# Optimization experiments

Hardware: AMD Instinct MI355X
Metric: run time of the kernel (lower is better)

## Reference

```python
import jax, jax.numpy as jnp
import numpy as np

D_MODEL = 1024
N_HEADS = 16
D_HEAD = D_MODEL // N_HEADS


def setup_inputs() -> dict:
    key = jax.random.key(0)
    k1, k2, k3 = jax.random.split(key, 3)
    B, T = 2, 2048
    x = jax.random.normal(k1, (B, T, D_MODEL), dtype=jnp.float32)
    # kaiming_normal fan_out on torch Linear weight [out, in]: std = sqrt(2/out)
    qkv_w = jax.random.normal(k2, (3 * D_MODEL, D_MODEL), dtype=jnp.float32) * np.sqrt(2.0 / (3 * D_MODEL)).astype(np.float32)
    out_w = jax.random.normal(k3, (D_MODEL, D_MODEL), dtype=jnp.float32) * np.sqrt(2.0 / D_MODEL).astype(np.float32)
    return {"x": x, "qkv_w": qkv_w, "out_w": out_w}


def rotate_half(x):
    x1, x2 = x[..., : x.shape[-1] // 2], x[..., x.shape[-1] // 2 :]
    return jnp.concatenate((-x2, x1), axis=-1)


def reference(x, qkv_w, out_w):
    B, T, D = x.shape
    H, dh = N_HEADS, D_HEAD
    scale = dh ** -0.5

    qkv = jnp.einsum('btd,ed->bte', x, qkv_w)  # [B,T,3D]
    q, k, v = jnp.split(qkv, 3, axis=-1)
    # [B,H,T,dh]
    q = q.reshape(B, T, H, dh).transpose(0, 2, 1, 3)
    k = k.reshape(B, T, H, dh).transpose(0, 2, 1, 3)
    v = v.reshape(B, T, H, dh).transpose(0, 2, 1, 3)

    # rotary embeddings
    inv_freq = 1.0 / (10000.0 ** (jnp.arange(0, dh, 2, dtype=jnp.float32) / dh))
    t = jnp.arange(T, dtype=jnp.float32)
    freqs = jnp.einsum('i,j->ij', t, inv_freq)        # [T, dh/2]
    emb = jnp.concatenate((freqs, freqs), axis=-1)    # [T, dh]
    cos = jnp.cos(emb)[None, None]                    # [1,1,T,dh]
    sin = jnp.sin(emb)[None, None]
    q = q * cos + rotate_half(q) * sin
    k = k * cos + rotate_half(k) * sin

    scores = jnp.einsum('bhqd,bhkd->bhqk', q, k) * scale
    causal = jnp.tril(jnp.ones((T, T), dtype=bool))
    scores = jnp.where(causal, scores, -jnp.inf)
    attn = jax.nn.softmax(scores, axis=-1)
    out = jnp.einsum('bhqk,bhkd->bhqd', attn, v)      # [B,H,T,dh]
    out = out.transpose(0, 2, 1, 3).reshape(B, T, D)
    return jnp.einsum('btd,ed->bte', out, out_w)
```

## Files before the change

kernel.cpp:

```cpp
#include <hip/hip_runtime.h>
#include <hip/hip_bf16.h>
#include <cmath>

#define Bb   2
#define Tseq 2048
#define NH   16
#define DM   1024

using f32x4 = __attribute__((ext_vector_type(4))) float;
using s16x8 = __attribute__((ext_vector_type(8))) short;
using s16x4 = __attribute__((ext_vector_type(4))) short;

typedef const __attribute__((address_space(1))) unsigned char* as1p;
typedef __attribute__((address_space(3))) unsigned char* as3p;

static __device__ __forceinline__ void gload_lds16(const void* g, void* l){
  __builtin_amdgcn_global_load_lds((as1p)g, (as3p)l, 16, 0, 0);
}

#if defined(__has_builtin)
#if __has_builtin(__builtin_amdgcn_mfma_f32_16x16x16bf16_1k)
#define MFMA16(acc, va, pb) (acc) = __builtin_amdgcn_mfma_f32_16x16x16bf16_1k((va), (pb), (acc), 0, 0, 0)
#endif
#endif
#ifndef MFMA16
#define MFMA16(acc, va, pb) asm volatile("s_nop 1\n\tv_mfma_f32_16x16x16_bf16 %0, %1, %2, %0" : "+v"(acc) : "v"(va), "v"(pb))
#endif

static __device__ __forceinline__ float b2f(unsigned short u){
  union { unsigned int u; float f; } v; v.u = ((unsigned int)u) << 16; return v.f;
}
static __device__ __forceinline__ unsigned short f2b(float f){
  union { float f; unsigned int u; } v; v.f = f;
  unsigned int u = v.u;
  return (unsigned short)((u + 0x7fffu + ((u >> 16) & 1u)) >> 16);
}

__global__ void k_convert(const float* __restrict__ in, unsigned short* __restrict__ out, int n){
  int stride = gridDim.x * blockDim.x;
  for (int i = blockIdx.x * blockDim.x + threadIdx.x; i * 4 < n; i += stride) {
    const float4 v = *reinterpret_cast<const float4*>(in + (size_t)i * 4);
    ushort4 o; o.x = f2b(v.x); o.y = f2b(v.y); o.z = f2b(v.z); o.w = f2b(v.w);
    *reinterpret_cast<ushort4*>(out + (size_t)i * 4) = o;
  }
}

__global__ void k_tables(float* __restrict__ cosT, float* __restrict__ sinT){
  int idx = blockIdx.x * blockDim.x + threadIdx.x;
  int t = idx >> 5, j = idx & 31;
  float invf = __powf(10000.0f, -(float)j / 32.0f);
  float a = (float)t * invf;
  cosT[idx] = cosf(a);
  sinT[idx] = sinf(a);
}

template<int OUT_BF16>
__global__ __launch_bounds__(256) void k_gemm_bt(const unsigned short* __restrict__ A,
                                                 const unsigned short* __restrict__ W,
                                                 void* __restrict__ Cout,
                                                 int M, int N, int K, int NYL){
  __shared__ unsigned short As[128*32];
  __shared__ unsigned short Bs[128*32];
  const int i = (int)blockIdx.x;
  const int xcd = i & 7, r = i >> 3;
  const int bx = r / NYL, by = xcd * NYL + (r % NYL);
  const int bm = bx * 128, bn = by * 128;
  const int tid = threadIdx.x;
  const int lane = tid & 63, w = tid >> 6;
  const int wr = w >> 1, wc = w & 1;
  const int g = lane >> 4, ln = lane & 15;
  f32x4 acc[4][4] = {};
  char* asb = (char*)As + w * 2048;
  char* bsb = (char*)Bs + w * 2048;
  const int lrow = lane >> 2;
  const int kcol = (lane & 3) * 8;
  const size_t aro = (size_t)(bm + w * 32 + lrow) * K;
  const size_t bro = (size_t)(bn + w * 32 + lrow) * K;
  for (int k0 = 0; k0 < K; k0 += 32) {
    gload_lds16(A + aro + k0 + kcol,                  asb);
    gload_lds16(A + aro + (size_t)16 * K + k0 + kcol, asb + 1024);
    gload_lds16(W + bro + k0 + kcol,                  bsb);
    gload_lds16(W + bro + (size_t)16 * K + k0 + kcol, bsb + 1024);
    __syncthreads();
    s16x8 af[4], bfr[4];
    #pragma unroll
    for (int mt = 0; mt < 4; ++mt)
      af[mt] = *reinterpret_cast<const s16x8*>(&As[(wr*64 + mt*16 + ln)*32 + g*8]);
    #pragma unroll
    for (int nt = 0; nt < 4; ++nt)
      bfr[nt] = *reinterpret_cast<const s16x8*>(&Bs[(wc*64 + nt*16 + ln)*32 + g*8]);
    #pragma unroll
    for (int mt = 0; mt < 4; ++mt)
      #pragma unroll
      for (int nt = 0; nt < 4; ++nt)
        acc[mt][nt] = __builtin_amdgcn_mfma_f32_16x16x32_bf16(af[mt], bfr[nt], acc[mt][nt], 0, 0, 0);
    __syncthreads();
  }
  #pragma unroll
  for (int mt = 0; mt < 4; ++mt)
    #pragma unroll
    for (int nt = 0; nt < 4; ++nt)
      #pragma unroll
      for (int r2 = 0; r2 < 4; ++r2) {
        int row = bm + wr*64 + mt*16 + g*4 + r2;
        int col = bn + wc*64 + nt*16 + ln;
        float vv = acc[mt][nt][r2];
        if (OUT_BF16) reinterpret_cast<unsigned short*>(Cout)[(size_t)row * N + col] = f2b(vv);
        else          reinterpret_cast<float*>(Cout)[(size_t)row * N + col] = vv;
      }
}

__global__ __launch_bounds__(256) void k_rope_split(const unsigned short* __restrict__ qkv,
                                                    const float* __restrict__ cosT,
                                                    const float* __restrict__ sinT,
                                                    unsigned short* __restrict__ qr,
                                                    unsigned short* __restrict__ kr){
  int bt = blockIdx.x;
  int b = bt / Tseq, t = bt % Tseq;
  const unsigned short* row = qkv + (size_t)bt * 3072;
  for (int d = threadIdx.x; d < 1024; d += 256) {
    int h = d >> 6, dd = d & 63;
    int j = dd & 31;
    float c = cosT[t*32 + j], s = sinT[t*32 + j];
    int part = (dd < 32) ? (d + 32) : (d - 32);
    float xq  = b2f(row[d]);
    float xq2 = b2f(row[part]);
    float qv = (dd < 32) ? (xq*c - xq2*s) : (xq*c + xq2*s);
    size_t head_off = ((size_t)(b*NH + h) * Tseq + t) * 64 + dd;
    qr[head_off] = f2b(qv * 0.125f);
    float xk  = b2f(row[1024 + d]);
    float xk2 = b2f(row[1024 + part]);
    float kv = (dd < 32) ? (xk*c - xk2*s) : (xk*c + xk2*s);
    kr[head_off] = f2b(kv);
  }
}

__global__ __launch_bounds__(256) void k_vtrans(const unsigned short* __restrict__ qkv,
                                                unsigned short* __restrict__ vt){
  __shared__ unsigned short L[64*72];
  const int blk = blockIdx.x;
  const int tt64 = blk & 31, bh = blk >> 5;
  const int b = bh >> 4, h = bh & 15;
  const int t0 = tt64 * 64;
  const int tid = threadIdx.x;
  {
    const int tr = tid >> 2, c = tid & 3;
    const unsigned short* src = qkv + ((size_t)(b * Tseq) + t0 + tr) * 3072 + 2048 + h * 64 + c * 16;
    uint4 a0 = *reinterpret_cast<const uint4*>(src);
    uint4 a1 = *reinterpret_cast<const uint4*>(src + 8);
    *reinterpret_cast<uint4*>(&L[tr * 72 + c * 16])     = a0;
    *reinterpret_cast<uint4*>(&L[tr * 72 + c * 16 + 8]) = a1;
  }
  __syncthreads();
  {
    const int d = tid >> 2, c = tid & 3;
    unsigned int wq[8];
    #pragma unroll
    for (int j = 0; j < 8; ++j) {
      unsigned int lo = L[(c * 16 + 2 * j)     * 72 + d];
      unsigned int hi = L[(c * 16 + 2 * j + 1) * 72 + d];
      wq[j] = lo | (hi << 16);
    }
    unsigned short* dst = vt + ((size_t)bh * 64 + d) * Tseq + t0 + c * 16;
    *reinterpret_cast<uint4*>(dst)     = make_uint4(wq[0], wq[1], wq[2], wq[3]);
    *reinterpret_cast<uint4*>(dst + 8) = make_uint4(wq[4], wq[5], wq[6], wq[7]);
  }
}

__global__ __launch_bounds__(256, 2) void k_attn(const unsigned short* __restrict__ Qr,
                                                 const unsigned short* __restrict__ Kr,
                                                 const unsigned short* __restrict__ Vt,
                                                 unsigned short* __restrict__ Ao){
  __shared__ unsigned short Ks[2][64*64];
  __shared__ unsigned short Vs[2][64*64];
  __shared__ unsigned short Ps[4][16*72];
  const int i = (int)blockIdx.x;
  const int xcd = i & 7, r = i >> 3;
  const int bh = xcd * 4 + (r >> 4);
  const int pj = r & 15;
  const unsigned short* Q  = Qr + (size_t)bh * Tseq * 64;
  const unsigned short* Kp = Kr + (size_t)bh * Tseq * 64;
  const unsigned short* Vp = Vt + (size_t)bh * 64 * Tseq;
  const int tid = threadIdx.x;
  const int w = tid >> 6, lane = tid & 63;
  const int g = lane >> 4, ln = lane & 15;
  const int srow = tid >> 2;
  const int c2 = (tid & 3) * 2;
  const int wb0 = srow * 128 + ((c2 * 16)        ^ ((srow & 7) << 4));
  const int wb1 = srow * 128 + ((c2 * 16 + 16)   ^ ((srow & 7) << 4));
  const int scol = c2 * 8;
  const int x0 = (g * 16)      ^ ((ln & 7) << 4);
  const int x1 = (64 + g * 16) ^ ((ln & 7) << 4);
  unsigned short* Pw = Ps[w];
  const int b = bh / NH, h = bh % NH;

  #pragma unroll
  for (int pass = 0; pass < 2; ++pass) {
    const int j = pass ? (31 - pj) : pj;
    const int q0 = j * 64;
    const int ntiles = j + 1;
    const int q0w = q0 + w * 16;

    s16x8 qf0 = *reinterpret_cast<const s16x8*>(&Q[(size_t)(q0w + ln) * 64 + g * 8]);
    s16x8 qf1 = *reinterpret_cast<const s16x8*>(&Q[(size_t)(q0w + ln) * 64 + 32 + g * 8]);

    f32x4 oacc[4] = {};
    float lsum = 0.f;

    {
      uint4 k0 = *reinterpret_cast<const uint4*>(&Kp[(size_t)srow * 64 + scol]);
      uint4 k1 = *reinterpret_cast<const uint4*>(&Kp[(size_t)srow * 64 + scol + 8]);
      uint4 v0 = *reinterpret_cast<const uint4*>(&Vp[(size_t)srow * Tseq + scol]);
      uint4 v1 = *reinterpret_cast<const uint4*>(&Vp[(size_t)srow * Tseq + scol + 8]);
      *reinterpret_cast<uint4*>((char*)Ks[0] + wb0) = k0;
      *reinterpret_cast<uint4*>((char*)Ks[0] + wb1) = k1;
      *reinterpret_cast<uint4*>((char*)Vs[0] + wb0) = v0;
      *reinterpret_cast<uint4*>((char*)Vs[0] + wb1) = v1;
    }
    __syncthreads();
    int cur = 0;

    for (int kt = 0; kt < ntiles; ++kt) {
      const bool pre = (kt + 1 < ntiles);
      uint4 nk0, nk1, nv0, nv1;
      if (pre) {
        const unsigned short* gk = &Kp[(size_t)((kt + 1) * 64 + srow) * 64 + scol];
        const unsigned short* gv = &Vp[(size_t)srow * Tseq + (kt + 1) * 64 + scol];
        nk0 = *reinterpret_cast<const uint4*>(gk);
        nk1 = *reinterpret_cast<const uint4*>(gk + 8);
        nv0 = *reinterpret_cast<const uint4*>(gv);
        nv1 = *reinterpret_cast<const uint4*>(gv + 8);
      }
      f32x4 s[4] = {};
      const char* kb = (const char*)Ks[cur];
      __builtin_amdgcn_s_setprio(1);
      #pragma unroll
      for (int nt = 0; nt < 4; ++nt) {
        s16x8 kfa = *reinterpret_cast<const s16x8*>(kb + nt * 2048 + ln * 128 + x0);
        s16x8 kfb = *reinterpret_cast<const s16x8*>(kb + nt * 2048 + ln * 128 + x1);
        s[nt] = __builtin_amdgcn_mfma_f32_16x16x32_bf16(kfa, qf0, s[nt], 0, 0, 0);
        s[nt] = __builtin_amdgcn_mfma_f32_16x16x32_bf16(kfb, qf1, s[nt], 0, 0, 0);
      }
      __builtin_amdgcn_s_setprio(0);
      if (kt == ntiles - 1) {
        #pragma unroll
        for (int nt = 0; nt < 4; ++nt)
          #pragma unroll
          for (int r2 = 0; r2 < 4; ++r2)
            if (nt * 16 + g * 4 + r2 > w * 16 + ln) s[nt][r2] = -1e30f;
      }
      s16x4 pb[4];
      #pragma unroll
      for (int nt = 0; nt < 4; ++nt)
        #pragma unroll
        for (int r2 = 0; r2 < 4; ++r2) {
          float p = __expf(s[nt][r2]);
          lsum += p;
          pb[nt][r2] = (short)f2b(p);
        }
      const char* vb = (const char*)Vs[cur];
      __builtin_amdgcn_s_setprio(1);
      #pragma unroll
      for (int dt = 0; dt < 4; ++dt) {
        #pragma unroll
        for (int nt = 0; nt < 4; ++nt) {
          s16x4 va = *reinterpret_cast<const s16x4*>(vb + (dt * 16 + ln) * 128 + ((nt * 32 + g * 8) ^ ((ln & 7) << 4)));
          MFMA16(oacc[dt], va, pb[nt]);
        }
      }
      __builtin_amdgcn_s_setprio(0);
      if (pre) {
        const int nxt = cur ^ 1;
        *reinterpret_cast<uint4*>((char*)Ks[nxt] + wb0) = nk0;
        *reinterpret_cast<uint4*>((char*)Ks[nxt] + wb1) = nk1;
        *reinterpret_cast<uint4*>((char*)Vs[nxt] + wb0) = nv0;
        *reinterpret_cast<uint4*>((char*)Vs[nxt] + wb1) = nv1;
      }
      __syncthreads();
      cur ^= 1;
    }

    float l = lsum;
    l += __shfl_xor(l, 16);
    l += __shfl_xor(l, 32);
    float inv = 1.f / l;
    #pragma unroll
    for (int nt = 0; nt < 4; ++nt) {
      unsigned int lo = (unsigned int)f2b(oacc[nt][0] * inv) | ((unsigned int)f2b(oacc[nt][1] * inv) << 16);
      unsigned int hi = (unsigned int)f2b(oacc[nt][2] * inv) | ((unsigned int)f2b(oacc[nt][3] * inv) << 16);
      *reinterpret_cast<uint2*>(&Pw[ln * 72 + nt * 16 + g * 4]) = make_uint2(lo, hi);
    }
    asm volatile("s_waitcnt lgkmcnt(0)" ::: "memory");
    __builtin_amdgcn_sched_barrier(0);
    const int rr = lane >> 2;
    const int cc = (lane & 3) * 8;
    uint4 ov0 = *reinterpret_cast<const uint4*>(&Pw[rr * 72 + cc]);
    uint4 ov1 = *reinterpret_cast<const uint4*>(&Pw[rr * 72 + cc + 32]);
    int t = q0w + rr;
    unsigned short* orow = &Ao[((size_t)(b * Tseq + t) * DM) + h * 64];
    *reinterpret_cast<uint4*>(orow + cc)      = ov0;
    *reinterpret_cast<uint4*>(orow + cc + 32) = ov1;
  }
}

extern "C" void kernel_launch(void* const* d_in, const int* in_sizes, int n_in,
                              void* d_out, int out_size, void* d_ws, size_t ws_size,
                              hipStream_t stream) {
  const float* x    = (const float*)d_in[0];
  const float* qkvw = (const float*)d_in[1];
  const float* outw = (const float*)d_in[2];
  float* out = (float*)d_out;
  char* ws = (char*)d_ws;
  size_t off = 0;
  auto alloc = [&](size_t bytes)->void*{ void* p = ws + off; off += (bytes + 255) & ~(size_t)255; return p; };
  unsigned short* x_bf   = (unsigned short*)alloc((size_t)Bb*Tseq*DM*2);
  unsigned short* qw_bf  = (unsigned short*)alloc((size_t)3*DM*DM*2);
  unsigned short* ow_bf  = (unsigned short*)alloc((size_t)DM*DM*2);
  float*          cosT   = (float*)alloc((size_t)Tseq*32*4);
  float*          sinT   = (float*)alloc((size_t)Tseq*32*4);
  unsigned short* qkv_bf = (unsigned short*)alloc((size_t)Bb*Tseq*3*DM*2);
  unsigned short* qr     = (unsigned short*)alloc((size_t)Bb*NH*Tseq*64*2);
  unsigned short* kr     = (unsigned short*)alloc((size_t)Bb*NH*Tseq*64*2);
  unsigned short* vt     = (unsigned short*)alloc((size_t)Bb*NH*Tseq*64*2);
  unsigned short* ao     = (unsigned short*)alloc((size_t)Bb*Tseq*DM*2);
  (void)ws_size; (void)in_sizes; (void)n_in; (void)out_size;

  const int nx  = Bb*Tseq*DM;
  const int nqw = 3*DM*DM;
  const int now = DM*DM;
  k_convert<<<2048, 256, 0, stream>>>(x, x_bf, nx);
  k_convert<<<2048, 256, 0, stream>>>(qkvw, qw_bf, nqw);
  k_convert<<<1024, 256, 0, stream>>>(outw, ow_bf, now);
  k_tables<<<256, 256, 0, stream>>>(cosT, sinT);
  k_gemm_bt<1><<<768, 256, 0, stream>>>(x_bf, qw_bf, qkv_bf, Bb*Tseq, 3*DM, DM, 3);
  k_rope_split<<<Bb*Tseq, 256, 0, stream>>>(qkv_bf, cosT, sinT, qr, kr);
  k_vtrans<<<Bb*NH*(Tseq/64), 256, 0, stream>>>(qkv_bf, vt);
  k_attn<<<dim3(Bb*NH*16), 256, 0, stream>>>(qr, kr, vt, ao);
  k_gemm_bt<0><<<256, 256, 0, stream>>>(ao, ow_bf, out, Bb*Tseq, DM, DM, 1);
}
```

Baseline: 131.3 us.

## Fuse RoPE and head split into QKV GEMM epilogue; deepen K tile with swizzled LDS

The QKV GEMM epilogue now applies rotary embedding, the Q scale and the per-head layout directly from accumulators. This removes the separate rope_split kernel and its extra read and write of the Q/K portion of the qkv buffer. Only the V region is still written to the qkv buffer. The GEMM K-step is also doubled to 64 with an XOR-swizzled LDS layout to cut barrier count and bank conflicts. In exchange, LDS use is doubled and the epilogue loads cos/sin tables per row.

```diff
diff --git a/kernel.cpp b/kernel.cpp
--- a/kernel.cpp
+++ b/kernel.cpp
@@ -54,84 +54,105 @@
   sinT[idx] = sinf(a);
 }
 
-template<int OUT_BF16>
+template<int MODE>
 __global__ __launch_bounds__(256) void k_gemm_bt(const unsigned short* __restrict__ A,
                                                  const unsigned short* __restrict__ W,
                                                  void* __restrict__ Cout,
-                                                 int M, int N, int K, int NYL){
-  __shared__ unsigned short As[128*32];
-  __shared__ unsigned short Bs[128*32];
+                                                 int M, int N, int K, int NYL,
+                                                 const float* __restrict__ cosT,
+                                                 const float* __restrict__ sinT,
+                                                 unsigned short* __restrict__ qr,
+                                                 unsigned short* __restrict__ kr){
+  __shared__ unsigned short As[128*64];
+  __shared__ unsigned short Bs[128*64];
   const int i = (int)blockIdx.x;
-  const int xcd = i & 7, r = i >> 3;
-  const int bx = r / NYL, by = xcd * NYL + (r % NYL);
+  const int xcd = i & 7, rr = i >> 3;
+  const int bx = rr / NYL, by = xcd * NYL + (rr % NYL);
   const int bm = bx * 128, bn = by * 128;
   const int tid = threadIdx.x;
   const int lane = tid & 63, w = tid >> 6;
   const int wr = w >> 1, wc = w & 1;
   const int g = lane >> 4, ln = lane & 15;
   f32x4 acc[4][4] = {};
-  char* asb = (char*)As + w * 2048;
-  char* bsb = (char*)Bs + w * 2048;
-  const int lrow = lane >> 2;
-  const int kcol = (lane & 3) * 8;
-  const size_t aro = (size_t)(bm + w * 32 + lrow) * K;
-  const size_t bro = (size_t)(bn + w * 32 + lrow) * K;
-  for (int k0 = 0; k0 < K; k0 += 32) {
-    gload_lds16(A + aro + k0 + kcol,                  asb);
-    gload_lds16(A + aro + (size_t)16 * K + k0 + kcol, asb + 1024);
-    gload_lds16(W + bro + k0 + kcol,                  bsb);
-    gload_lds16(W + bro + (size_t)16 * K + k0 + kcol, bsb + 1024);
+  char* asb = (char*)As + w * 4096;
+  char* bsb = (char*)Bs + w * 4096;
+  const int lrow8 = lane >> 3;
+  const int kcolb = ((lane & 7) ^ lrow8) * 16;
+  const size_t aro = (size_t)(bm + w * 32 + lrow8) * K;
+  const size_t bro = (size_t)(bn + w * 32 + lrow8) * K;
+  const int xr = (ln & 7) << 4;
+  for (int k0 = 0; k0 < K; k0 += 64) {
+    #pragma unroll
+    for (int q4 = 0; q4 < 4; ++q4) {
+      gload_lds16((const char*)(A + aro + (size_t)(q4 * 8) * K + k0) + kcolb, asb + q4 * 1024);
+      gload_lds16((const char*)(W + bro + (size_t)(q4 * 8) * K + k0) + kcolb, bsb + q4 * 1024);
+    }
     __syncthreads();
-    s16x8 af[4], bfr[4];
+    #pragma unroll
+    for (int kk = 0; kk < 2; ++kk) {
+      s16x8 af[4], bfr[4];
+      const int ro = (kk * 64 + g * 16) ^ xr;
+      #pragma unroll
+      for (int mt = 0; mt < 4; ++mt)
+        af[mt] = *reinterpret_cast<const s16x8*>((char*)As + (wr*64 + mt*16 + ln) * 128 + ro);
+      #pragma unroll
+      for (int nt = 0; nt < 4; ++nt)
+        bfr[nt] = *reinterpret_cast<const s16x8*>((char*)Bs + (wc*64 + nt*16 + ln) * 128 + ro);
+      #pragma unroll
+      for (int mt = 0; mt < 4; ++mt)
+        #pragma unroll
+        for (int nt = 0; nt < 4; ++nt)
+          acc[mt][nt] = __builtin_amdgcn_mfma_f32_16x16x32_bf16(af[mt], bfr[nt], acc[mt][nt], 0, 0, 0);
+    }
+    __syncthreads();
+  }
+  if (MODE == 0) {
     #pragma unroll
     for (int mt = 0; mt < 4; ++mt)
-      af[mt] = *reinterpret_cast<const s16x8*>(&As[(wr*64 + mt*16 + ln)*32 + g*8]);
-    #pragma unroll
-    for (int nt = 0; nt < 4; ++nt)
-      bfr[nt] = *reinterpret_cast<const s16x8*>(&Bs[(wc*64 + nt*16 + ln)*32 + g*8]);
-    #pragma unroll
-    for (int mt = 0; mt < 4; ++mt)
       #pragma unroll
       for (int nt = 0; nt < 4; ++nt)
-        acc[mt][nt] = __builtin_amdgcn_mfma_f32_16x16x32_bf16(af[mt], bfr[nt], acc[mt][nt], 0, 0, 0);
-    __syncthreads();
-  }
-  #pragma unroll
-  for (int mt = 0; mt < 4; ++mt)
-    #pragma unroll
-    for (int nt = 0; nt < 4; ++nt)
-      #pragma unroll
-      for (int r2 = 0; r2 < 4; ++r2) {
-        int row = bm + wr*64 + mt*16 + g*4 + r2;
-        int col = bn + wc*64 + nt*16 + ln;
-        float vv = acc[mt][nt][r2];
-        if (OUT_BF16) reinterpret_cast<unsigned short*>(Cout)[(size_t)row * N + col] = f2b(vv);
-        else          reinterpret_cast<float*>(Cout)[(size_t)row * N + col] = vv;
-      }
-}
-
-__global__ __launch_bounds__(256) void k_rope_split(const unsigned short* __restrict__ qkv,
-                                                    const float* __restrict__ cosT,
-                                                    const float* __restrict__ sinT,
-                                                    unsigned short* __restrict__ qr,
-                                                    unsigned short* __restrict__ kr){
-  int bt = blockIdx.x;
-  int b = bt / Tseq, t = bt % Tseq;
-  const unsigned short* row = qkv + (size_t)bt * 3072;
-  for (int d = threadIdx.x; d < 1024; d += 256) {
-    int h = d >> 6, dd = d & 63;
-    int j = dd & 31;
-    float c = cosT[t*32 + j], s = sinT[t*32 + j];
-    int part = (dd < 32) ? (d + 32) : (d - 32);
-    float xq  = b2f(row[d]);
-    float xq2 = b2f(row[part]);
-    float qv = (dd < 32) ? (xq*c - xq2*s) : (xq*c + xq2*s);
-    size_t head_off = ((size_t)(b*NH + h) * Tseq + t) * 64 + dd;
-    qr[head_off] = f2b(qv * 0.125f);
-    float xk  = b2f(row[1024 + d]);
-    float xk2 = b2f(row[1024 + part]);
-    float kv = (dd < 32) ? (xk*c - xk2*s) : (xk*c + xk2*s);
-    kr[head_off] = f2b(kv);
+        #pragma unroll
+        for (int r = 0; r < 4; ++r) {
+          int row = bm + wr*64 + mt*16 + g*4 + r;
+          int col = bn + wc*64 + nt*16 + ln;
+          reinterpret_cast<float*>(Cout)[(size_t)row * N + col] = acc[mt][nt][r];
+        }
+  } else {
+    const int region = bn >> 10;
+    if (region == 2) {
+      #pragma unroll
+      for (int mt = 0; mt < 4; ++mt)
+        #pragma unroll
+        for (int nt = 0; nt < 4; ++nt)
+          #pragma unroll
+          for (int r = 0; r < 4; ++r) {
+            int row = bm + wr*64 + mt*16 + g*4 + r;
+            int col = bn + wc*64 + nt*16 + ln;
+            reinterpret_cast<unsigned short*>(Cout)[(size_t)row * N + col] = f2b(acc[mt][nt][r]);
+          }
+    } else {
+      const int h = ((bn + wc * 64) >> 6) & 15;
+      unsigned short* dst = (region == 0) ? qr : kr;
+      const float qs = (region == 0) ? 0.125f : 1.0f;
+      #pragma unroll
+      for (int mt = 0; mt < 4; ++mt)
+        #pragma unroll
+        for (int r = 0; r < 4; ++r) {
+          int row = bm + wr*64 + mt*16 + g*4 + r;
+          int t = row & (Tseq - 1), b = row >> 11;
+          float c0 = cosT[t*32 + ln],      s0 = sinT[t*32 + ln];
+          float c1 = cosT[t*32 + 16 + ln], s1 = sinT[t*32 + 16 + ln];
+          float v0 = (acc[mt][0][r] * c0 - acc[mt][2][r] * s0) * qs;
+          float v1 = (acc[mt][1][r] * c1 - acc[mt][3][r] * s1) * qs;
+          float v2 = (acc[mt][2][r] * c0 + acc[mt][0][r] * s0) * qs;
+          float v3 = (acc[mt][3][r] * c1 + acc[mt][1][r] * s1) * qs;
+          size_t base = ((size_t)(b * NH + h) * Tseq + t) * 64 + ln;
+          dst[base]      = f2b(v0);
+          dst[base + 16] = f2b(v1);
+          dst[base + 32] = f2b(v2);
+          dst[base + 48] = f2b(v3);
+        }
+    }
   }
 }
 
@@ -332,9 +353,10 @@
   k_convert<<<2048, 256, 0, stream>>>(qkvw, qw_bf, nqw);
   k_convert<<<1024, 256, 0, stream>>>(outw, ow_bf, now);
   k_tables<<<256, 256, 0, stream>>>(cosT, sinT);
-  k_gemm_bt<1><<<768, 256, 0, stream>>>(x_bf, qw_bf, qkv_bf, Bb*Tseq, 3*DM, DM, 3);
-  k_rope_split<<<Bb*Tseq, 256, 0, stream>>>(qkv_bf, cosT, sinT, qr, kr);
+  k_gemm_bt<2><<<768, 256, 0, stream>>>(x_bf, qw_bf, qkv_bf, Bb*Tseq, 3*DM, DM, 3,
+                                        cosT, sinT, qr, kr);
   k_vtrans<<<Bb*NH*(Tseq/64), 256, 0, stream>>>(qkv_bf, vt);
   k_attn<<<dim3(Bb*NH*16), 256, 0, stream>>>(qr, kr, vt, ao);
-  k_gemm_bt<0><<<256, 256, 0, stream>>>(ao, ow_bf, out, Bb*Tseq, DM, DM, 1);
-}
+  k_gemm_bt<0><<<256, 256, 0, stream>>>(ao, ow_bf, out, Bb*Tseq, DM, DM, 1,
+                                        cosT, sinT, qr, kr);
+}
```

Result: faster. 124.2 us (-5.4%).
